# Kernel tuning notes

Hardware: AMD Instinct MI355X
Metric: run time of the kernel (lower is better)

## Reference

```python
import jax, jax.numpy as jnp
import numpy as np
from math import sqrt


def setup_inputs() -> dict:
    key = jax.random.key(0)
    ks = jax.random.split(key, 10)
    N, C = 192, 96  # C = N // 2
    n, h, w = 8, 64, 64
    s = lambda fan_in: 1.0 / np.sqrt(fan_in)
    return {
        "x": jax.random.normal(ks[0], (n, N, h, w), dtype=jnp.float32),
        "pe": jax.random.normal(ks[1], (N, 120, 120), dtype=jnp.float32) * 0.02,
        "wq": jax.random.normal(ks[2], (C, N), dtype=jnp.float32) * s(N),
        "bq": jax.random.normal(ks[3], (C,), dtype=jnp.float32) * 0.01,
        "wk": jax.random.normal(ks[4], (C, N), dtype=jnp.float32) * s(N),
        "bk": jax.random.normal(ks[5], (C,), dtype=jnp.float32) * 0.01,
        "wv": jax.random.normal(ks[6], (C, N), dtype=jnp.float32) * s(N),
        "bv": jax.random.normal(ks[7], (C,), dtype=jnp.float32) * 0.01,
        "wz": jax.random.normal(ks[8], (N, C), dtype=jnp.float32) * s(C),
        "bz": jax.random.normal(ks[9], (N,), dtype=jnp.float32) * 0.01,
    }


def _conv1x1(x, w, b):
    # x: [n, cin, h, w]; w: [cout, cin]; b: [cout]
    return jnp.einsum("oc,nchw->nohw", w, x) + b[None, :, None, None]


def reference(x, pe, wq, bq, wk, bk, wv, bv, wz, bz):
    n, c_in, h, w = x.shape
    hw = h * w
    # 2D positional encoding, sliced to the actual spatial size
    x = x + pe[None, :, :h, :w]
    c = wq.shape[0]  # N // 2
    q = _conv1x1(x, wq, bq).reshape(n, c, hw)   # [n, c, hw]
    k = _conv1x1(x, wk, bk).reshape(n, c, hw)   # [n, c, hw]
    v = _conv1x1(x, wv, bv).reshape(n, c, hw)   # [n, c, hw]
    scale = sqrt(hw)
    # logits[n, i, j] = sum_c q[n,c,i] * k[n,c,j]
    logits = jnp.einsum("nci,ncj->nij", q, k) / scale  # [n, hw, hw]
    weights = jax.nn.softmax(logits, axis=-1)
    # z[n, c, i] = sum_j weights[n,i,j] * v[n,c,j]
    z = jnp.einsum("nij,ncj->nci", weights, v).reshape(n, c, h, w)
    z = _conv1x1(z, wz, bz)  # [n, N, h, w]
    return x + z
```

## Files before the change

kernel.cpp:

```cpp
#include <hip/hip_runtime.h>
#include <hip/hip_bf16.h>

#define HW 4096
#define CIN 192
#define CMID 96

typedef __attribute__((ext_vector_type(8))) short bf16x8;
typedef __attribute__((ext_vector_type(4))) float f32x4;
typedef __attribute__((ext_vector_type(16))) float f32x16;
typedef __attribute__((ext_vector_type(4))) unsigned int u32x4;
typedef __attribute__((ext_vector_type(2))) unsigned int u32x2;

static __device__ __forceinline__ unsigned short f2bf(float f) {
    union { float f; unsigned int u; } v;
    v.f = f;
    unsigned int r = v.u + 0x7fffu + ((v.u >> 16) & 1u);
    return (unsigned short)(r >> 16);
}

static __device__ __forceinline__ void gload16(const void* g, void* l) {
    __builtin_amdgcn_global_load_lds(
        (const __attribute__((address_space(1))) unsigned int*)g,
        (__attribute__((address_space(3))) unsigned int*)l, 16, 0, 0);
}

#define SCQ (0.015625f * 1.44269504089f)

__global__ __launch_bounds__(256) void convw_kernel(
    const float* __restrict__ wq, const float* __restrict__ wk,
    const float* __restrict__ wv, const float* __restrict__ wz,
    unsigned short* __restrict__ wqkvb, unsigned short* __restrict__ wzb)
{
    int idx = blockIdx.x * 256 + threadIdx.x;
    if (idx < 3 * CMID * CIN) {
        int m = idx / (CMID * CIN), r = idx % (CMID * CIN);
        const float* w = (m == 0) ? wq : ((m == 1) ? wk : wv);
        wqkvb[idx] = f2bf(w[r]);
    } else if (idx < 3 * CMID * CIN + CIN * CMID) {
        int r = idx - 3 * CMID * CIN;
        wzb[r] = f2bf(wz[r]);
    }
}

__global__ __launch_bounds__(512) void qkv_kernel(
    const float* __restrict__ x, const float* __restrict__ pe,
    const unsigned short* __restrict__ wqkvb,
    const float* __restrict__ bq, const float* __restrict__ bk,
    const float* __restrict__ bv,
    unsigned short* __restrict__ Q, unsigned short* __restrict__ K,
    unsigned short* __restrict__ V)
{
    const int bid = blockIdx.x;
    const int n = bid & 7, bx = bid >> 3;
    const int i0 = bx * 64, t = threadIdx.x;
    __shared__ unsigned short xt[64 * 200];

    #pragma unroll
    for (int it = 0; it < 2; ++it) {
        int u = t + it * 512;
        if (u < 768) {
            int c0 = (u >> 4) * 4, p0 = (u & 15) * 4;
            float a[4][4];
            #pragma unroll
            for (int cc = 0; cc < 4; ++cc) {
                f32x4 xv = *(const f32x4*)(x + ((size_t)n * CIN + c0 + cc) * HW + i0 + p0);
                f32x4 pv = *(const f32x4*)(pe + (c0 + cc) * 14400 + bx * 120 + p0);
                #pragma unroll
                for (int p = 0; p < 4; ++p) a[cc][p] = xv[p] + pv[p];
            }
            #pragma unroll
            for (int p = 0; p < 4; ++p) {
                unsigned w0, w1;
                asm("v_cvt_pk_bf16_f32 %0, %1, %2" : "=v"(w0) : "v"(a[0][p]), "v"(a[1][p]));
                asm("v_cvt_pk_bf16_f32 %0, %1, %2" : "=v"(w1) : "v"(a[2][p]), "v"(a[3][p]));
                u32x2 wv2 = {w0, w1};
                *(u32x2*)(xt + (p0 + p) * 200 + c0) = wv2;
            }
        }
    }
    __syncthreads();

    const int w = t >> 6, lane = t & 63, l15 = lane & 15, lg = lane >> 4;
    const int wg = w >> 2;
    const int p0 = (w & 3) * 16;

    bf16x8 af[6];
    #pragma unroll
    for (int f = 0; f < 6; ++f)
        af[f] = *(const bf16x8*)(xt + (p0 + l15) * 200 + f * 32 + lg * 8);

    #pragma unroll
    for (int cc = 0; cc < 9; ++cc) {
        const int ct = wg * 9 + cc;
        const int m = ct / 6, c6 = ct % 6;
        f32x4 acc = (f32x4){0.f, 0.f, 0.f, 0.f};
        const unsigned short* wrow = wqkvb + (ct * 16 + l15) * CIN + lg * 8;
        #pragma unroll
        for (int f = 0; f < 6; ++f) {
            bf16x8 wf = *(const bf16x8*)(wrow + f * 32);
            if (m < 2)
                acc = __builtin_amdgcn_mfma_f32_16x16x32_bf16(wf, af[f], acc, 0, 0, 0);
            else
                acc = __builtin_amdgcn_mfma_f32_16x16x32_bf16(af[f], wf, acc, 0, 0, 0);
        }
        if (m < 2) {
            f32x4 bv4 = *(const f32x4*)(((m == 0) ? bq : bk) + c6 * 16 + lg * 4);
            ushort4 pk4;
            if (m == 0) {
                pk4.x = f2bf((acc[0] + bv4[0]) * SCQ);
                pk4.y = f2bf((acc[1] + bv4[1]) * SCQ);
                pk4.z = f2bf((acc[2] + bv4[2]) * SCQ);
                pk4.w = f2bf((acc[3] + bv4[3]) * SCQ);
            } else {
                pk4.x = f2bf(acc[0] + bv4[0]);
                pk4.y = f2bf(acc[1] + bv4[1]);
                pk4.z = f2bf(acc[2] + bv4[2]);
                pk4.w = f2bf(acc[3] + bv4[3]);
            }
            unsigned short* dst = ((m == 0) ? Q : K) + (size_t)n * HW * CMID;
            *(ushort4*)(dst + (size_t)(i0 + p0 + l15) * CMID + c6 * 16 + lg * 4) = pk4;
        } else {
            const float bias = bv[c6 * 16 + l15];
            ushort4 pk4;
            pk4.x = f2bf(acc[0] + bias); pk4.y = f2bf(acc[1] + bias);
            pk4.z = f2bf(acc[2] + bias); pk4.w = f2bf(acc[3] + bias);
            *(ushort4*)(V + (size_t)n * CMID * HW + (size_t)(c6 * 16 + l15) * HW
                          + i0 + p0 + lg * 4) = pk4;
        }
    }
}

__global__ __launch_bounds__(256, 2) void attn_kernel(
    const unsigned short* __restrict__ Q, const unsigned short* __restrict__ K,
    const unsigned short* __restrict__ V,
    unsigned short* __restrict__ zp, float* __restrict__ lp)
{
    const int bid = blockIdx.x;
    const int n    = bid & 7;
    const int iblk = (bid >> 3) & 15;
    const int js   = bid >> 7;

    const int t = threadIdx.x, w = t >> 6, lane = t & 63;
    const int l31 = lane & 31, hi = lane >> 5;
    const int ib = iblk * 256 + w * 64;

    __shared__ unsigned short Ks[3][32 * 128];
    __shared__ unsigned short Vs[2][96 * 64];

    const unsigned short* Qb = Q + (size_t)n * HW * CMID;
    const unsigned short* Kb = K + (size_t)n * HW * CMID;
    const unsigned short* Vb = V + (size_t)n * CMID * HW;

    bf16x8 qf[2][6];
    #pragma unroll
    for (int is = 0; is < 2; ++is)
        #pragma unroll
        for (int kc = 0; kc < 6; ++kc)
            qf[is][kc] = *(const bf16x8*)(Qb + (size_t)(ib + is * 32 + l31) * CMID
                                            + kc * 16 + hi * 8);

    int ksoff[2], vsoff[3];
    #pragma unroll
    for (int s = 0; s < 2; ++s) {
        int row = 8 * w + 4 * s + (lane >> 4);
        ksoff[s] = row * CMID + (((lane & 15) ^ (row & 7)) * 8);
    }
    #pragma unroll
    for (int s = 0; s < 3; ++s) {
        int c = 8 * (w * 3 + s) + (lane >> 3);
        vsoff[s] = c * HW + (((lane & 7) ^ (c & 7)) * 8);
    }

    const int j00 = js * 1024;

#define STAGE_K(TILE, KB) do {                                                 \
    _Pragma("unroll") for (int s = 0; s < 2; ++s)                              \
        gload16(Kb + (size_t)(j00 + (TILE) * 32) * CMID + ksoff[s],            \
                &Ks[KB][(w * 2 + s) * 512]);                                   \
} while (0)
#define STAGE_V(WND, VB) do {                                                  \
    _Pragma("unroll") for (int s = 0; s < 3; ++s)                              \
        gload16(Vb + (size_t)(j00 + (WND) * 64) + vsoff[s],                    \
                &Vs[VB][(w * 3 + s) * 512]);                                   \
} while (0)

    f32x16 O[2][3], Lon[2];
    #pragma unroll
    for (int is = 0; is < 2; ++is) {
        #pragma unroll
        for (int cc = 0; cc < 3; ++cc)
            #pragma unroll
            for (int e = 0; e < 16; ++e) O[is][cc][e] = 0.f;
        #pragma unroll
        for (int e = 0; e < 16; ++e) Lon[is][e] = 0.f;
    }

    bf16x8 onef;
    #pragma unroll
    for (int e = 0; e < 8; ++e) onef[e] = (short)0x3F80;

    STAGE_K(0, 0);
    STAGE_K(1, 1);
    STAGE_V(0, 0);
    asm volatile("s_waitcnt vmcnt(0)" ::: "memory");
    __builtin_amdgcn_s_barrier();

#define BODY(KBUF, VBUF, VHALF) do {                                           \
    const unsigned short* Kc = &Ks[KBUF][0];                                   \
    const unsigned short* Vc = &Vs[VBUF][0];                                   \
    f32x16 s0, s1;                                                             \
    _Pragma("unroll") for (int e = 0; e < 16; ++e) { s0[e] = 0.f; s1[e] = 0.f; } \
    __builtin_amdgcn_s_setprio(1);                                             \
    _Pragma("unroll") for (int kc = 0; kc < 6; ++kc) {                         \
        bf16x8 kf = *(const bf16x8*)(Kc + l31 * 128 +                          \
                      (((kc * 2 + hi) ^ (l31 & 7)) << 3));                     \
        s0 = __builtin_amdgcn_mfma_f32_32x32x16_bf16(kf, qf[0][kc], s0, 0, 0, 0); \
        s1 = __builtin_amdgcn_mfma_f32_32x32x16_bf16(kf, qf[1][kc], s1, 0, 0, 0); \
    }                                                                          \
    __builtin_amdgcn_s_setprio(0);                                             \
    unsigned pkk[2][4][2];                                                     \
    _Pragma("unroll") for (int q = 0; q < 4; ++q)                              \
        _Pragma("unroll") for (int rp = 0; rp < 2; ++rp) {                     \
            float lo0 = __builtin_exp2f(s0[q * 4 + 2 * rp]);                   \
            float hh0 = __builtin_exp2f(s0[q * 4 + 2 * rp + 1]);               \
            float lo1 = __builtin_exp2f(s1[q * 4 + 2 * rp]);                   \
            float hh1 = __builtin_exp2f(s1[q * 4 + 2 * rp + 1]);               \
            asm("v_cvt_pk_bf16_f32 %0, %1, %2"                                 \
                : "=v"(pkk[0][q][rp]) : "v"(lo0), "v"(hh0));                   \
            asm("v_cvt_pk_bf16_f32 %0, %1, %2"                                 \
                : "=v"(pkk[1][q][rp]) : "v"(lo1), "v"(hh1));                   \
        }                                                                      \
    u32x4 pfu[2][2];                                                           \
    _Pragma("unroll") for (int is = 0; is < 2; ++is)                           \
        _Pragma("unroll") for (int jc = 0; jc < 2; ++jc) {                     \
            unsigned x0 = pkk[is][2 * jc][0], y0 = pkk[is][2 * jc + 1][0];     \
            unsigned x1 = pkk[is][2 * jc][1], y1 = pkk[is][2 * jc + 1][1];     \
            asm("v_permlane32_swap_b32 %0, %1" : "+v"(y0), "+v"(x0));          \
            asm("v_permlane32_swap_b32 %0, %1" : "+v"(y1), "+v"(x1));          \
            pfu[is][jc][0] = x0; pfu[is][jc][1] = x1;                          \
            pfu[is][jc][2] = y0; pfu[is][jc][3] = y1;                          \
        }                                                                      \
    __builtin_amdgcn_s_setprio(1);                                             \
    _Pragma("unroll") for (int jc = 0; jc < 2; ++jc) {                         \
        bf16x8 pa0 = __builtin_bit_cast(bf16x8, pfu[0][jc]);                   \
        bf16x8 pa1 = __builtin_bit_cast(bf16x8, pfu[1][jc]);                   \
        _Pragma("unroll") for (int cc = 0; cc < 3; ++cc) {                     \
            bf16x8 vf = *(const bf16x8*)(Vc + (cc * 32 + l31) * 64 +           \
                          ((((VHALF) * 4 + jc * 2 + hi) ^ (l31 & 7)) << 3));   \
            O[0][cc] = __builtin_amdgcn_mfma_f32_32x32x16_bf16(pa0, vf, O[0][cc], 0, 0, 0); \
            O[1][cc] = __builtin_amdgcn_mfma_f32_32x32x16_bf16(pa1, vf, O[1][cc], 0, 0, 0); \
        }                                                                      \
        Lon[0] = __builtin_amdgcn_mfma_f32_32x32x16_bf16(pa0, onef, Lon[0], 0, 0, 0); \
        Lon[1] = __builtin_amdgcn_mfma_f32_32x32x16_bf16(pa1, onef, Lon[1], 0, 0, 0); \
    }                                                                          \
    __builtin_amdgcn_s_setprio(0);                                             \
} while (0)

    int kb = 0, kb1 = 1, kb2 = 2;
    for (int tt = 0; tt < 32; tt += 2) {
        {
            const int pfk = (tt + 2 < 32) ? tt + 2 : 31;
            STAGE_K(pfk, kb2);
            const int wn = (tt >> 1) + 1;
            const int pfw = (wn < 16) ? wn : 15;
            STAGE_V(pfw, wn & 1);
            BODY(kb, (tt >> 1) & 1, 0);
            asm volatile("s_waitcnt vmcnt(5)" ::: "memory");
            __builtin_amdgcn_s_barrier();
        }
        {
            const int pfk = (tt + 3 < 32) ? tt + 3 : 31;
            STAGE_K(pfk, kb);
            BODY(kb1, (tt >> 1) & 1, 1);
            asm volatile("s_waitcnt vmcnt(2)" ::: "memory");
            __builtin_amdgcn_s_barrier();
        }
        const int tmp = kb;
        kb = kb2; kb2 = kb1; kb1 = tmp;
    }
#undef BODY
#undef STAGE_K
#undef STAGE_V

    asm volatile("s_waitcnt vmcnt(0)" ::: "memory");

    unsigned short* zb = zp + ((size_t)js * 8 + n) * HW * CMID;
    #pragma unroll
    for (int is = 0; is < 2; ++is)
        #pragma unroll
        for (int cc = 0; cc < 3; ++cc)
            #pragma unroll
            for (int r = 0; r < 16; ++r) {
                int i = ib + is * 32 + (r & 3) + 8 * (r >> 2) + 4 * hi;
                zb[(size_t)i * CMID + cc * 32 + l31] = f2bf(O[is][cc][r]);
            }

    if (l31 == 0) {
        float* lb = lp + ((size_t)js * 8 + n) * HW;
        #pragma unroll
        for (int is = 0; is < 2; ++is)
            #pragma unroll
            for (int r = 0; r < 16; ++r) {
                int i = ib + is * 32 + (r & 3) + 8 * (r >> 2) + 4 * hi;
                lb[i] = Lon[is][r];
            }
    }
}

__global__ __launch_bounds__(256) void zproj_kernel(
    const unsigned short* __restrict__ zp, const float* __restrict__ lp,
    const unsigned short* __restrict__ wzb, const float* __restrict__ bz,
    const float* __restrict__ x, const float* __restrict__ pe,
    float* __restrict__ out)
{
    const int bid = blockIdx.x;
    const int n = bid & 7, bx = bid >> 3;
    const int i0 = bx * 64, t = threadIdx.x;
    __shared__ unsigned short zt[64 * 104];
    __shared__ float ll[64];

    if (t < 64) {
        float s = 0.f;
        #pragma unroll
        for (int sl = 0; sl < 4; ++sl)
            s += lp[(size_t)sl * 8 * HW + (size_t)n * HW + i0 + t];
        ll[t] = 1.f / s;
    }
    __syncthreads();

    #pragma unroll
    for (int u = 0; u < 3; ++u) {
        int unit = t + u * 256;
        int i = unit / 12, g = unit % 12;
        size_t gidx = ((size_t)n * HW + i0 + i) * CMID + g * 8;
        float a[8];
        #pragma unroll
        for (int e = 0; e < 8; ++e) a[e] = 0.f;
        #pragma unroll
        for (int sl = 0; sl < 4; ++sl) {
            u32x4 wv = *(const u32x4*)(zp + (size_t)sl * 8 * HW * CMID + gidx);
            #pragma unroll
            for (int k = 0; k < 4; ++k) {
                union { unsigned u; float f; } lo, hi2;
                lo.u = wv[k] << 16;
                hi2.u = wv[k] & 0xffff0000u;
                a[2 * k]     += lo.f;
                a[2 * k + 1] += hi2.f;
            }
        }
        float li = ll[i];
        unsigned ww[4];
        #pragma unroll
        for (int k = 0; k < 4; ++k) {
            float p0 = a[2 * k] * li, p1 = a[2 * k + 1] * li;
            asm("v_cvt_pk_bf16_f32 %0, %1, %2" : "=v"(ww[k]) : "v"(p0), "v"(p1));
        }
        u32x4 wv4 = {ww[0], ww[1], ww[2], ww[3]};
        *(u32x4*)(zt + i * 104 + g * 8) = wv4;
    }
    __syncthreads();

    const int w = t >> 6, lane = t & 63, l15 = lane & 15, lg = lane >> 4;
    const int p0 = w * 16;

    bf16x8 af[3];
    #pragma unroll
    for (int f = 0; f < 3; ++f)
        af[f] = *(const bf16x8*)(zt + (p0 + l15) * 104 + f * 32 + lg * 8);

    #pragma unroll
    for (int ct = 0; ct < 12; ++ct) {
        f32x4 acc = (f32x4){0.f, 0.f, 0.f, 0.f};
        const unsigned short* wrow = wzb + (ct * 16 + l15) * CMID + lg * 8;
        #pragma unroll
        for (int f = 0; f < 3; ++f) {
            bf16x8 wf = *(const bf16x8*)(wrow + f * 32);
            acc = __builtin_amdgcn_mfma_f32_16x16x32_bf16(af[f], wf, acc, 0, 0, 0);
        }
        const int co = ct * 16 + l15;
        const int ibase = i0 + p0 + lg * 4;
        size_t xa = ((size_t)n * CIN + co) * HW + ibase;
        f32x4 xv = *(const f32x4*)(x + xa);
        f32x4 pv = *(const f32x4*)(pe + co * 14400 + bx * 120 + p0 + lg * 4);
        const float bias = bz[co];
        f32x4 o;
        #pragma unroll
        for (int r = 0; r < 4; ++r) o[r] = xv[r] + pv[r] + acc[r] + bias;
        *(f32x4*)(out + xa) = o;
    }
}

extern "C" void kernel_launch(void* const* d_in, const int* in_sizes, int n_in,
                              void* d_out, int out_size, void* d_ws, size_t ws_size,
                              hipStream_t stream) {
    const float* x  = (const float*)d_in[0];
    const float* pe = (const float*)d_in[1];
    const float* wq = (const float*)d_in[2];
    const float* bq = (const float*)d_in[3];
    const float* wk = (const float*)d_in[4];
    const float* bk = (const float*)d_in[5];
    const float* wv = (const float*)d_in[6];
    const float* bv = (const float*)d_in[7];
    const float* wz = (const float*)d_in[8];
    const float* bz = (const float*)d_in[9];
    float* out = (float*)d_out;

    char* ws = (char*)d_ws;
    unsigned short* wqkvb = (unsigned short*)(ws);
    unsigned short* wzb   = (unsigned short*)(ws + 131072);
    unsigned short* Qb    = (unsigned short*)(ws + 196608);
    unsigned short* Kb    = (unsigned short*)(ws + 6488064);
    unsigned short* Vb    = (unsigned short*)(ws + 12779520);
    unsigned short* zpb   = (unsigned short*)(ws + 19070976);
    float*          lpb   = (float*)(ws + 44236800);

    convw_kernel<<<288, 256, 0, stream>>>(wq, wk, wv, wz, wqkvb, wzb);
    qkv_kernel<<<512, 512, 0, stream>>>(x, pe, wqkvb, bq, bk, bv, Qb, Kb, Vb);
    attn_kernel<<<512, 256, 0, stream>>>(Qb, Kb, Vb, zpb, lpb);
    zproj_kernel<<<512, 256, 0, stream>>>(zpb, lpb, wzb, bz, x, pe, out);
}
```

Before: 131.8 us.

## Halve attention row tile per wave and double grid for higher occupancy

Each wave in the attention kernel now handles 32 query rows instead of 64. The grid doubles to 1024 blocks and the launch bounds request 4 blocks per SIMD. K staging drops from triple to double buffering, and each tile's loads are now fully drained with vmcnt(0) before the barrier. The goal is to cut register and LDS pressure so more waves can hide latency. The cost is half the reuse of each K/V tile loaded into LDS, twice the global K/V traffic, and a shallower prefetch pipeline.

```diff
diff --git a/kernel.cpp b/kernel.cpp
--- a/kernel.cpp
+++ b/kernel.cpp
@@ -130,39 +130,36 @@
     }
 }
 
-__global__ __launch_bounds__(256, 2) void attn_kernel(
+__global__ __launch_bounds__(256, 4) void attn_kernel(
     const unsigned short* __restrict__ Q, const unsigned short* __restrict__ K,
     const unsigned short* __restrict__ V,
     unsigned short* __restrict__ zp, float* __restrict__ lp)
 {
     const int bid = blockIdx.x;
     const int n    = bid & 7;
-    const int iblk = (bid >> 3) & 15;
-    const int js   = bid >> 7;
+    const int iblk = (bid >> 3) & 31;
+    const int js   = bid >> 8;
 
     const int t = threadIdx.x, w = t >> 6, lane = t & 63;
     const int l31 = lane & 31, hi = lane >> 5;
-    const int ib = iblk * 256 + w * 64;
-
-    __shared__ unsigned short Ks[3][32 * 128];
+    const int ib = iblk * 128 + w * 32;
+
+    __shared__ unsigned short Ks[2][32 * 128];
     __shared__ unsigned short Vs[2][96 * 64];
 
     const unsigned short* Qb = Q + (size_t)n * HW * CMID;
     const unsigned short* Kb = K + (size_t)n * HW * CMID;
     const unsigned short* Vb = V + (size_t)n * CMID * HW;
 
-    bf16x8 qf[2][6];
-    #pragma unroll
-    for (int is = 0; is < 2; ++is)
-        #pragma unroll
-        for (int kc = 0; kc < 6; ++kc)
-            qf[is][kc] = *(const bf16x8*)(Qb + (size_t)(ib + is * 32 + l31) * CMID
-                                            + kc * 16 + hi * 8);
+    bf16x8 qf[6];
+    #pragma unroll
+    for (int kc = 0; kc < 6; ++kc)
+        qf[kc] = *(const bf16x8*)(Qb + (size_t)(ib + l31) * CMID + kc * 16 + hi * 8);
 
     int ksoff[2], vsoff[3];
     #pragma unroll
     for (int s = 0; s < 2; ++s) {
-        int row = 8 * w + 4 * s + (lane >> 4);
+        int row = 4 * (w * 2 + s) + (lane >> 4);
         ksoff[s] = row * CMID + (((lane & 15) ^ (row & 7)) * 8);
     }
     #pragma unroll
@@ -184,23 +181,15 @@
                 &Vs[VB][(w * 3 + s) * 512]);                                   \
 } while (0)
 
-    f32x16 O[2][3], Lon[2];
-    #pragma unroll
-    for (int is = 0; is < 2; ++is) {
-        #pragma unroll
-        for (int cc = 0; cc < 3; ++cc)
-            #pragma unroll
-            for (int e = 0; e < 16; ++e) O[is][cc][e] = 0.f;
-        #pragma unroll
-        for (int e = 0; e < 16; ++e) Lon[is][e] = 0.f;
-    }
+    f32x16 O[3], Lon;
+    #pragma unroll
+    for (int e = 0; e < 16; ++e) { O[0][e] = 0.f; O[1][e] = 0.f; O[2][e] = 0.f; Lon[e] = 0.f; }
 
     bf16x8 onef;
     #pragma unroll
     for (int e = 0; e < 8; ++e) onef[e] = (short)0x3F80;
 
     STAGE_K(0, 0);
-    STAGE_K(1, 1);
     STAGE_V(0, 0);
     asm volatile("s_waitcnt vmcnt(0)" ::: "memory");
     __builtin_amdgcn_s_barrier();
@@ -208,102 +197,83 @@
 #define BODY(KBUF, VBUF, VHALF) do {                                           \
     const unsigned short* Kc = &Ks[KBUF][0];                                   \
     const unsigned short* Vc = &Vs[VBUF][0];                                   \
-    f32x16 s0, s1;                                                             \
-    _Pragma("unroll") for (int e = 0; e < 16; ++e) { s0[e] = 0.f; s1[e] = 0.f; } \
+    f32x16 sacc;                                                               \
+    _Pragma("unroll") for (int e = 0; e < 16; ++e) sacc[e] = 0.f;              \
     __builtin_amdgcn_s_setprio(1);                                             \
     _Pragma("unroll") for (int kc = 0; kc < 6; ++kc) {                         \
         bf16x8 kf = *(const bf16x8*)(Kc + l31 * 128 +                          \
                       (((kc * 2 + hi) ^ (l31 & 7)) << 3));                     \
-        s0 = __builtin_amdgcn_mfma_f32_32x32x16_bf16(kf, qf[0][kc], s0, 0, 0, 0); \
-        s1 = __builtin_amdgcn_mfma_f32_32x32x16_bf16(kf, qf[1][kc], s1, 0, 0, 0); \
+        sacc = __builtin_amdgcn_mfma_f32_32x32x16_bf16(kf, qf[kc], sacc, 0, 0, 0); \
     }                                                                          \
     __builtin_amdgcn_s_setprio(0);                                             \
-    unsigned pkk[2][4][2];                                                     \
+    unsigned pkk[4][2];                                                        \
     _Pragma("unroll") for (int q = 0; q < 4; ++q)                              \
         _Pragma("unroll") for (int rp = 0; rp < 2; ++rp) {                     \
-            float lo0 = __builtin_exp2f(s0[q * 4 + 2 * rp]);                   \
-            float hh0 = __builtin_exp2f(s0[q * 4 + 2 * rp + 1]);               \
-            float lo1 = __builtin_exp2f(s1[q * 4 + 2 * rp]);                   \
-            float hh1 = __builtin_exp2f(s1[q * 4 + 2 * rp + 1]);               \
+            float lo = __builtin_exp2f(sacc[q * 4 + 2 * rp]);                  \
+            float hh = __builtin_exp2f(sacc[q * 4 + 2 * rp + 1]);              \
             asm("v_cvt_pk_bf16_f32 %0, %1, %2"                                 \
-                : "=v"(pkk[0][q][rp]) : "v"(lo0), "v"(hh0));                   \
-            asm("v_cvt_pk_bf16_f32 %0, %1, %2"                                 \
-                : "=v"(pkk[1][q][rp]) : "v"(lo1), "v"(hh1));                   \
+                : "=v"(pkk[q][rp]) : "v"(lo), "v"(hh));                        \
         }                                                                      \
-    u32x4 pfu[2][2];                                                           \
-    _Pragma("unroll") for (int is = 0; is < 2; ++is)                           \
-        _Pragma("unroll") for (int jc = 0; jc < 2; ++jc) {                     \
-            unsigned x0 = pkk[is][2 * jc][0], y0 = pkk[is][2 * jc + 1][0];     \
-            unsigned x1 = pkk[is][2 * jc][1], y1 = pkk[is][2 * jc + 1][1];     \
-            asm("v_permlane32_swap_b32 %0, %1" : "+v"(y0), "+v"(x0));          \
-            asm("v_permlane32_swap_b32 %0, %1" : "+v"(y1), "+v"(x1));          \
-            pfu[is][jc][0] = x0; pfu[is][jc][1] = x1;                          \
-            pfu[is][jc][2] = y0; pfu[is][jc][3] = y1;                          \
-        }                                                                      \
+    u32x4 pfu[2];                                                              \
+    _Pragma("unroll") for (int jc = 0; jc < 2; ++jc) {                         \
+        unsigned x0 = pkk[2 * jc][0], y0 = pkk[2 * jc + 1][0];                 \
+        unsigned x1 = pkk[2 * jc][1], y1 = pkk[2 * jc + 1][1];                 \
+        asm("v_permlane32_swap_b32 %0, %1" : "+v"(y0), "+v"(x0));              \
+        asm("v_permlane32_swap_b32 %0, %1" : "+v"(y1), "+v"(x1));              \
+        pfu[jc][0] = x0; pfu[jc][1] = x1;                                      \
+        pfu[jc][2] = y0; pfu[jc][3] = y1;                                      \
+    }                                                                          \
     __builtin_amdgcn_s_setprio(1);                                             \
     _Pragma("unroll") for (int jc = 0; jc < 2; ++jc) {                         \
-        bf16x8 pa0 = __builtin_bit_cast(bf16x8, pfu[0][jc]);                   \
-        bf16x8 pa1 = __builtin_bit_cast(bf16x8, pfu[1][jc]);                   \
+        bf16x8 pa = __builtin_bit_cast(bf16x8, pfu[jc]);                       \
         _Pragma("unroll") for (int cc = 0; cc < 3; ++cc) {                     \
             bf16x8 vf = *(const bf16x8*)(Vc + (cc * 32 + l31) * 64 +           \
                           ((((VHALF) * 4 + jc * 2 + hi) ^ (l31 & 7)) << 3));   \
-            O[0][cc] = __builtin_amdgcn_mfma_f32_32x32x16_bf16(pa0, vf, O[0][cc], 0, 0, 0); \
-            O[1][cc] = __builtin_amdgcn_mfma_f32_32x32x16_bf16(pa1, vf, O[1][cc], 0, 0, 0); \
+            O[cc] = __builtin_amdgcn_mfma_f32_32x32x16_bf16(pa, vf, O[cc], 0, 0, 0); \
         }                                                                      \
-        Lon[0] = __builtin_amdgcn_mfma_f32_32x32x16_bf16(pa0, onef, Lon[0], 0, 0, 0); \
-        Lon[1] = __builtin_amdgcn_mfma_f32_32x32x16_bf16(pa1, onef, Lon[1], 0, 0, 0); \
+        Lon = __builtin_amdgcn_mfma_f32_32x32x16_bf16(pa, onef, Lon, 0, 0, 0); \
     }                                                                          \
     __builtin_amdgcn_s_setprio(0);                                             \
 } while (0)
 
-    int kb = 0, kb1 = 1, kb2 = 2;
     for (int tt = 0; tt < 32; tt += 2) {
         {
-            const int pfk = (tt + 2 < 32) ? tt + 2 : 31;
-            STAGE_K(pfk, kb2);
+            STAGE_K(tt + 1, (tt + 1) & 1);
             const int wn = (tt >> 1) + 1;
             const int pfw = (wn < 16) ? wn : 15;
             STAGE_V(pfw, wn & 1);
-            BODY(kb, (tt >> 1) & 1, 0);
-            asm volatile("s_waitcnt vmcnt(5)" ::: "memory");
+            BODY(tt & 1, (tt >> 1) & 1, 0);
+            asm volatile("s_waitcnt vmcnt(3)" ::: "memory");
             __builtin_amdgcn_s_barrier();
         }
         {
-            const int pfk = (tt + 3 < 32) ? tt + 3 : 31;
-            STAGE_K(pfk, kb);
-            BODY(kb1, (tt >> 1) & 1, 1);
-            asm volatile("s_waitcnt vmcnt(2)" ::: "memory");
+            const int pfk = (tt + 2 < 32) ? tt + 2 : 31;
+            STAGE_K(pfk, (tt + 2) & 1);
+            BODY((tt + 1) & 1, (tt >> 1) & 1, 1);
+            asm volatile("s_waitcnt vmcnt(0)" ::: "memory");
             __builtin_amdgcn_s_barrier();
         }
-        const int tmp = kb;
-        kb = kb2; kb2 = kb1; kb1 = tmp;
     }
 #undef BODY
 #undef STAGE_K
 #undef STAGE_V
 
-    asm volatile("s_waitcnt vmcnt(0)" ::: "memory");
-
     unsigned short* zb = zp + ((size_t)js * 8 + n) * HW * CMID;
     #pragma unroll
-    for (int is = 0; is < 2; ++is)
-        #pragma unroll
-        for (int cc = 0; cc < 3; ++cc)
-            #pragma unroll
-            for (int r = 0; r < 16; ++r) {
-                int i = ib + is * 32 + (r & 3) + 8 * (r >> 2) + 4 * hi;
-                zb[(size_t)i * CMID + cc * 32 + l31] = f2bf(O[is][cc][r]);
-            }
+    for (int cc = 0; cc < 3; ++cc)
+        #pragma unroll
+        for (int r = 0; r < 16; ++r) {
+            int i = ib + (r & 3) + 8 * (r >> 2) + 4 * hi;
+            zb[(size_t)i * CMID + cc * 32 + l31] = f2bf(O[cc][r]);
+        }
 
     if (l31 == 0) {
         float* lb = lp + ((size_t)js * 8 + n) * HW;
         #pragma unroll
-        for (int is = 0; is < 2; ++is)
-            #pragma unroll
-            for (int r = 0; r < 16; ++r) {
-                int i = ib + is * 32 + (r & 3) + 8 * (r >> 2) + 4 * hi;
-                lb[i] = Lon[is][r];
-            }
+        for (int r = 0; r < 16; ++r) {
+            int i = ib + (r & 3) + 8 * (r >> 2) + 4 * hi;
+            lb[i] = Lon[r];
+        }
     }
 }
 
@@ -416,6 +386,6 @@
 
     convw_kernel<<<288, 256, 0, stream>>>(wq, wk, wv, wz, wqkvb, wzb);
     qkv_kernel<<<512, 512, 0, stream>>>(x, pe, wqkvb, bq, bk, bv, Qb, Kb, Vb);
-    attn_kernel<<<512, 256, 0, stream>>>(Qb, Kb, Vb, zpb, lpb);
+    attn_kernel<<<1024, 256, 0, stream>>>(Qb, Kb, Vb, zpb, lpb);
     zproj_kernel<<<512, 256, 0, stream>>>(zpb, lpb, wzb, bz, x, pe, out);
 }
```

Result: slower. 170.3 us (+29.2%).
